# Kernel tuning notes

Hardware: AMD Instinct MI355X
Metric: run time of the kernel (lower is better)

The kernel has to match this reference:

```python
import jax, jax.numpy as jnp
import numpy as np
import math


def _per_component_log_likelihood(x, MU, A, D, PI):
    # x: [N,d]; MU,D: [K,d]; A: [K,d,l]; PI: [K]
    K, d, l = A.shape
    iD = D ** (-2.0)                                   # [K,d]  (1/sigma^2 per feature)
    B = iD[:, :, None] * A                             # [K,d,l] = diag(iD_k) @ A_k
    # L_k = I_l + A_k^T diag(iD_k) A_k  (Woodbury inner matrix)
    L = jnp.eye(l, dtype=x.dtype)[None] + jnp.einsum('kdl,kdm->klm', A, B)
    iL = jnp.linalg.inv(L)                             # [K,l,l]
    # Mahalanobis term m_d[n,k] = xc^T iD xc - (xc^T iD A) iL (A^T iD xc),
    # expanded so we never materialize the [K,N,d] centered tensor.
    t_quad = (x * x) @ iD.T                            # [N,K]
    t_cross = x @ (iD * MU).T                          # [N,K]
    t_const = jnp.sum(iD * MU * MU, axis=1)            # [K]
    term1 = t_quad - 2.0 * t_cross + t_const[None, :]
    y = jnp.einsum('nd,kdl->nkl', x, B) - jnp.einsum('kd,kdl->kl', MU, B)[None]
    term2 = jnp.einsum('nkl,klm,nkm->nk', y, iL, y)
    m_d = term1 - term2                                # [N,K]
    # log|Sigma_k| = log|L_k| - sum_d log iD[k,d]
    log_det_Sigma = jnp.log(jnp.linalg.det(L)) + jnp.sum(jnp.log(D ** 2.0), axis=1)
    log_prob = -0.5 * ((d * math.log(2.0 * math.pi) + log_det_Sigma)[None, :] + m_d)
    # NOTE: faithful to the source, which adds PI (not log PI) here.
    return PI[None, :] + log_prob                      # [N,K]


def setup_inputs() -> dict:
    key = jax.random.key(0)
    k1, k2, k3, k4 = jax.random.split(key, 4)
    N, K, d, l = 500000, 32, 128, 4
    x = jax.random.normal(k1, (N, d), dtype=jnp.float32)
    MU = jax.random.normal(k2, (K, d), dtype=jnp.float32)
    A = 0.1 * jax.random.normal(k3, (K, d, l), dtype=jnp.float32)
    D = jax.random.uniform(k4, (K, d), dtype=jnp.float32, minval=0.5, maxval=1.5)
    PI = jnp.ones((K,), dtype=jnp.float32) / K
    return {"x": x, "MU": MU, "A": A, "D": D, "PI": PI}


def reference(x, MU, A, D, PI):
    comp_ll = _per_component_log_likelihood(x, MU, A, D, PI)   # [N,K]
    return jax.scipy.special.logsumexp(comp_ll, axis=1)        # [N] = MFA.log_prob(x)
```

## Files before the change

kernel.cpp:

```cpp
#include <hip/hip_runtime.h>
#include <hip/hip_bf16.h>

typedef _Float16 half8 __attribute__((ext_vector_type(8)));
typedef float f32x4 __attribute__((ext_vector_type(4)));

#define KC 32
#define DD 128
#define LL 4
#define NCOL 192
#define NBLK 768

__global__ __launch_bounds__(256) void mfa_precompute(
    const float* __restrict__ MU, const float* __restrict__ A,
    const float* __restrict__ D, const float* __restrict__ PI,
    _Float16* __restrict__ wsw, float* __restrict__ wsc, float* __restrict__ wsh)
{
  __shared__ float sPart[KC][8][16];
  __shared__ float sRi[KC][LL][LL];
  const int tid = threadIdx.x;
  const int k = tid >> 3;
  const int sub = tid & 7;

  {
    float p[16];
#pragma unroll
    for (int i = 0; i < 16; ++i) p[i] = 0.f;
    const int d0 = sub * 16;
    for (int di = 0; di < 16; ++di) {
      const int d = d0 + di;
      const float Dv = D[k*DD + d];
      const float id = 1.0f/(Dv*Dv);
      const float mu = MU[k*DD + d];
      float a[LL];
#pragma unroll
      for (int l = 0; l < LL; ++l) a[l] = A[(k*DD + d)*LL + l];
      int s = 0;
#pragma unroll
      for (int l = 0; l < LL; ++l) {
#pragma unroll
        for (int m2 = 0; m2 <= l; ++m2) { p[s] += a[l]*id*a[m2]; ++s; }
        p[10 + l] += mu*id*a[l];
      }
      p[14] += id*mu*mu;
      p[15] += logf(Dv*Dv);
    }
#pragma unroll
    for (int i = 0; i < 16; ++i) sPart[k][sub][i] = p[i];
  }
  __syncthreads();

  if (tid < KC) {
    const int kk = tid;
    float p[16];
#pragma unroll
    for (int i = 0; i < 16; ++i) p[i] = 0.f;
    for (int s = 0; s < 8; ++s)
#pragma unroll
      for (int i = 0; i < 16; ++i) p[i] += sPart[kk][s][i];

    float Lm[LL][LL];
    {
      int s = 0;
      for (int l = 0; l < LL; ++l)
        for (int m2 = 0; m2 <= l; ++m2) { Lm[l][m2] = p[s]; ++s; }
    }
    for (int l = 0; l < LL; ++l) Lm[l][l] += 1.0f;
    float c[LL];
    for (int l = 0; l < LL; ++l) c[l] = p[10 + l];
    const float t_const  = p[14];
    const float sumlogD2 = p[15];

    float Lo[LL][LL];
    for (int i = 0; i < LL; ++i)
      for (int j = 0; j < LL; ++j) Lo[i][j] = 0.f;
    for (int i = 0; i < LL; ++i) {
      float s = Lm[i][i];
      for (int m2 = 0; m2 < i; ++m2) s -= Lo[i][m2]*Lo[i][m2];
      Lo[i][i] = sqrtf(s);
      for (int j = i + 1; j < LL; ++j) {
        float t = Lm[j][i];
        for (int m2 = 0; m2 < i; ++m2) t -= Lo[j][m2]*Lo[i][m2];
        Lo[j][i] = t / Lo[i][i];
      }
    }
    float Ri[LL][LL];
    for (int i = 0; i < LL; ++i)
      for (int j = 0; j < LL; ++j) Ri[i][j] = 0.f;
    for (int i = 0; i < LL; ++i) {
      Ri[i][i] = 1.0f/Lo[i][i];
      for (int j = 0; j < i; ++j) {
        float s = 0.f;
        for (int m2 = j; m2 < i; ++m2) s += Lo[i][m2]*Ri[m2][j];
        Ri[i][j] = -s / Lo[i][i];
      }
    }
    for (int i = 0; i < LL; ++i)
      for (int j = 0; j < LL; ++j) sRi[kk][i][j] = Ri[i][j];
    for (int l = 0; l < LL; ++l) {
      float s = 0.f;
      for (int m2 = 0; m2 <= l; ++m2) s += Ri[l][m2]*c[m2];
      wsh[kk*LL + l] = s;
    }
    float logdetL = 0.f;
    for (int i = 0; i < LL; ++i) logdetL += logf(Lo[i][i]);
    logdetL *= 2.0f;
    const float dlog2pi = 235.24826473f;
    wsc[kk] = PI[kk] - 0.5f*(dlog2pi + logdetL + sumlogD2) - 0.5f*t_const;
  }
  __syncthreads();

  for (int idx = tid; idx < NCOL*DD; idx += blockDim.x) {
    const int j8   = idx & 7;
    const int lane = (idx >> 3) & 63;
    const int s    = (idx >> 9) & 3;
    const int t    = idx >> 11;
    const int col  = t*16 + (lane & 15);
    const int dd   = s*32 + ((lane >> 4) << 3) + j8;
    float v;
    if (col < 32) {
      const float Dv = D[col*DD + dd];
      v = 1.0f/(Dv*Dv);
    } else if (col < 64) {
      const int kk = col - 32;
      const float Dv = D[kk*DD + dd];
      v = MU[kk*DD + dd]/(Dv*Dv);
    } else {
      const int kk = (col - 64) >> 2, l = (col - 64) & 3;
      const float Dv = D[kk*DD + dd];
      const float id = 1.0f/(Dv*Dv);
      float s2 = 0.f;
      for (int m2 = 0; m2 <= l; ++m2) s2 += A[(kk*DD + dd)*LL + m2]*sRi[kk][l][m2];
      v = id*s2;
    }
    wsw[idx] = (_Float16)v;
  }
}

__global__ __launch_bounds__(256, 3) void mfa_main(
    const float* __restrict__ x, const _Float16* __restrict__ wsw,
    const float* __restrict__ wsc, const float* __restrict__ wsh,
    float* __restrict__ out, int N, int ntiles, int iters)
{
  __shared__ int4 sWbuf[3072];
  const int tid = threadIdx.x;

  {
    const int4* src = (const int4*)wsw;
    for (int i = tid; i < 3072; i += 256) sWbuf[i] = src[i];
  }

  const half8* sW8 = (const half8*)sWbuf;
  const int wv = tid >> 6, lane = tid & 63;
  const int m = lane & 15, g = lane >> 4;
  const int q = m >> 2;
  const int gbase = lane & 48;

  const float c0 = wsc[m];
  const float c1 = wsc[16 + m];
  float hh[8];
#pragma unroll
  for (int j = 0; j < 8; ++j) hh[j] = wsh[j*16 + m];

  __syncthreads();

  for (int it = 0; it < iters; ++it) {
    const int tile = it*(NBLK*4) + (int)blockIdx.x*4 + wv;
    if (tile >= ntiles) continue;

    const int row = tile*16 + m;
    const float* xr = x + (size_t)row*DD + g*8;
    half8 ax[4], ax2[4];
#pragma unroll
    for (int s = 0; s < 4; ++s) {
      const float4 v0 = *(const float4*)(xr + s*32);
      const float4 v1 = *(const float4*)(xr + s*32 + 4);
      half8 h, h2;
      h[0] = (_Float16)v0.x; h[1] = (_Float16)v0.y;
      h[2] = (_Float16)v0.z; h[3] = (_Float16)v0.w;
      h[4] = (_Float16)v1.x; h[5] = (_Float16)v1.y;
      h[6] = (_Float16)v1.z; h[7] = (_Float16)v1.w;
      h2[0] = (_Float16)(v0.x*v0.x); h2[1] = (_Float16)(v0.y*v0.y);
      h2[2] = (_Float16)(v0.z*v0.z); h2[3] = (_Float16)(v0.w*v0.w);
      h2[4] = (_Float16)(v1.x*v1.x); h2[5] = (_Float16)(v1.y*v1.y);
      h2[6] = (_Float16)(v1.z*v1.z); h2[7] = (_Float16)(v1.w*v1.w);
      ax[s] = h; ax2[s] = h2;
    }

    f32x4 acc[12];
#pragma unroll
    for (int t = 0; t < 12; ++t)
#pragma unroll
      for (int r = 0; r < 4; ++r) acc[t][r] = 0.f;

#pragma unroll
    for (int s = 0; s < 4; ++s) {
#pragma unroll
      for (int t = 0; t < 12; ++t) {
        const half8 b = sW8[(t*4 + s)*64 + lane];
        acc[t] = __builtin_amdgcn_mfma_f32_16x16x32_f16(
            (t < 2) ? ax2[s] : ax[s], b, acc[t], 0, 0, 0);
      }
    }

    float vp0[4], vp1[4];
#pragma unroll
    for (int r = 0; r < 4; ++r) {
      vp0[r] = acc[2][r] - 0.5f*acc[0][r] + c0;
      vp1[r] = acc[3][r] - 0.5f*acc[1][r] + c1;
    }
    float t2[8][4];
#pragma unroll
    for (int j = 0; j < 8; ++j)
#pragma unroll
      for (int r = 0; r < 4; ++r) {
        float e = acc[j + 4][r] - hh[j];
        e = e*e;
        e += __shfl_xor(e, 1);
        e += __shfl_xor(e, 2);
        t2[j][r] = e;
      }
    float res[4];
#pragma unroll
    for (int r = 0; r < 4; ++r) {
      float v[8];
#pragma unroll
      for (int jj = 0; jj < 4; ++jj) {
        const int src = gbase + 4*jj + q;
        v[jj]     = __shfl(vp0[r], src) + 0.5f*t2[jj][r];
        v[jj + 4] = __shfl(vp1[r], src) + 0.5f*t2[jj + 4][r];
      }
      float mx = v[0];
#pragma unroll
      for (int i = 1; i < 8; ++i) mx = fmaxf(mx, v[i]);
      mx = fmaxf(mx, __shfl_xor(mx, 4));
      mx = fmaxf(mx, __shfl_xor(mx, 8));
      float sum = 0.f;
#pragma unroll
      for (int i = 0; i < 8; ++i) sum += __expf(v[i] - mx);
      sum += __shfl_xor(sum, 4);
      sum += __shfl_xor(sum, 8);
      res[r] = mx + __logf(sum);
    }
    if (m == 0) {
      float4 o; o.x = res[0]; o.y = res[1]; o.z = res[2]; o.w = res[3];
      *(float4*)(out + (size_t)tile*16 + g*4) = o;
    }
  }
}

extern "C" void kernel_launch(void* const* d_in, const int* in_sizes, int n_in,
                              void* d_out, int out_size, void* d_ws, size_t ws_size,
                              hipStream_t stream) {
  const float* x  = (const float*)d_in[0];
  const float* MU = (const float*)d_in[1];
  const float* A  = (const float*)d_in[2];
  const float* D  = (const float*)d_in[3];
  const float* PI = (const float*)d_in[4];
  float* out = (float*)d_out;

  const int N = in_sizes[0] / DD;
  _Float16* wsw = (_Float16*)d_ws;
  float* wsc = (float*)((char*)d_ws + (size_t)NCOL*DD*sizeof(_Float16));
  float* wsh = wsc + KC;

  hipLaunchKernelGGL(mfa_precompute, dim3(1), dim3(256), 0, stream,
                     MU, A, D, PI, wsw, wsc, wsh);

  const int ntiles = (N + 15) / 16;
  const int iters  = (ntiles + NBLK*4 - 1) / (NBLK*4);
  hipLaunchKernelGGL(mfa_main, dim3(NBLK), dim3(256), 0, stream,
                     x, wsw, wsc, wsh, out, N, ntiles, iters);
}
```

Measured before the change: 401.6 us.

## Prefetch next x tile in registers and parallelize weight precompute across blocks

```diff
diff --git a/kernel.cpp b/kernel.cpp
--- a/kernel.cpp
+++ b/kernel.cpp
@@ -9,14 +9,14 @@
 #define LL 4
 #define NCOL 192
 #define NBLK 768
-
-__global__ __launch_bounds__(256) void mfa_precompute(
+#define NSLOT (NBLK*4)
+
+__global__ __launch_bounds__(256) void mfa_woodbury(
     const float* __restrict__ MU, const float* __restrict__ A,
     const float* __restrict__ D, const float* __restrict__ PI,
-    _Float16* __restrict__ wsw, float* __restrict__ wsc, float* __restrict__ wsh)
+    float* __restrict__ wsc, float* __restrict__ wsh, float* __restrict__ wsr)
 {
   __shared__ float sPart[KC][8][16];
-  __shared__ float sRi[KC][LL][LL];
   const int tid = threadIdx.x;
   const int k = tid >> 3;
   const int sub = tid & 7;
@@ -26,6 +26,7 @@
 #pragma unroll
     for (int i = 0; i < 16; ++i) p[i] = 0.f;
     const int d0 = sub * 16;
+#pragma unroll 4
     for (int di = 0; di < 16; ++di) {
       const int d = d0 + di;
       const float Dv = D[k*DD + d];
@@ -42,7 +43,7 @@
         p[10 + l] += mu*id*a[l];
       }
       p[14] += id*mu*mu;
-      p[15] += logf(Dv*Dv);
+      p[15] += __logf(Dv*Dv);
     }
 #pragma unroll
     for (int i = 0; i < 16; ++i) sPart[k][sub][i] = p[i];
@@ -95,45 +96,50 @@
       }
     }
     for (int i = 0; i < LL; ++i)
-      for (int j = 0; j < LL; ++j) sRi[kk][i][j] = Ri[i][j];
+      for (int j = 0; j < LL; ++j) wsr[kk*16 + i*4 + j] = Ri[i][j];
     for (int l = 0; l < LL; ++l) {
       float s = 0.f;
       for (int m2 = 0; m2 <= l; ++m2) s += Ri[l][m2]*c[m2];
       wsh[kk*LL + l] = s;
     }
     float logdetL = 0.f;
-    for (int i = 0; i < LL; ++i) logdetL += logf(Lo[i][i]);
+    for (int i = 0; i < LL; ++i) logdetL += __logf(Lo[i][i]);
     logdetL *= 2.0f;
     const float dlog2pi = 235.24826473f;
     wsc[kk] = PI[kk] - 0.5f*(dlog2pi + logdetL + sumlogD2) - 0.5f*t_const;
   }
-  __syncthreads();
-
-  for (int idx = tid; idx < NCOL*DD; idx += blockDim.x) {
-    const int j8   = idx & 7;
-    const int lane = (idx >> 3) & 63;
-    const int s    = (idx >> 9) & 3;
-    const int t    = idx >> 11;
-    const int col  = t*16 + (lane & 15);
-    const int dd   = s*32 + ((lane >> 4) << 3) + j8;
-    float v;
-    if (col < 32) {
-      const float Dv = D[col*DD + dd];
-      v = 1.0f/(Dv*Dv);
-    } else if (col < 64) {
-      const int kk = col - 32;
-      const float Dv = D[kk*DD + dd];
-      v = MU[kk*DD + dd]/(Dv*Dv);
-    } else {
-      const int kk = (col - 64) >> 2, l = (col - 64) & 3;
-      const float Dv = D[kk*DD + dd];
-      const float id = 1.0f/(Dv*Dv);
-      float s2 = 0.f;
-      for (int m2 = 0; m2 <= l; ++m2) s2 += A[(kk*DD + dd)*LL + m2]*sRi[kk][l][m2];
-      v = id*s2;
-    }
-    wsw[idx] = (_Float16)v;
-  }
+}
+
+__global__ __launch_bounds__(256) void mfa_weights(
+    const float* __restrict__ MU, const float* __restrict__ A,
+    const float* __restrict__ D, const float* __restrict__ wsr,
+    _Float16* __restrict__ wsw)
+{
+  const int idx = (int)blockIdx.x*256 + (int)threadIdx.x;
+  const int j8   = idx & 7;
+  const int lane = (idx >> 3) & 63;
+  const int s    = (idx >> 9) & 3;
+  const int t    = idx >> 11;
+  const int col  = t*16 + (lane & 15);
+  const int dd   = s*32 + ((lane >> 4) << 3) + j8;
+  float v;
+  if (col < 32) {
+    const float Dv = D[col*DD + dd];
+    v = 1.0f/(Dv*Dv);
+  } else if (col < 64) {
+    const int kk = col - 32;
+    const float Dv = D[kk*DD + dd];
+    v = MU[kk*DD + dd]/(Dv*Dv);
+  } else {
+    const int kk = (col - 64) >> 2, l = (col - 64) & 3;
+    const float Dv = D[kk*DD + dd];
+    const float id = 1.0f/(Dv*Dv);
+    float s2 = 0.f;
+    for (int m2 = 0; m2 <= l; ++m2)
+      s2 += A[(kk*DD + dd)*LL + m2] * wsr[kk*16 + l*4 + m2];
+    v = id*s2;
+  }
+  wsw[idx] = (_Float16)v;
 }
 
 __global__ __launch_bounds__(256, 3) void mfa_main(
@@ -163,17 +169,42 @@
 
   __syncthreads();
 
+  int tile = (int)blockIdx.x*4 + wv;
+  const int tmax = ntiles - 1;
+
+  float4 xv[8];
+  {
+    const int t0 = tile < ntiles ? tile : tmax;
+    const float* xr = x + (size_t)(t0*16 + m)*DD + g*8;
+#pragma unroll
+    for (int s = 0; s < 4; ++s) {
+      xv[2*s]     = *(const float4*)(xr + s*32);
+      xv[2*s + 1] = *(const float4*)(xr + s*32 + 4);
+    }
+  }
+
   for (int it = 0; it < iters; ++it) {
-    const int tile = it*(NBLK*4) + (int)blockIdx.x*4 + wv;
-    if (tile >= ntiles) continue;
-
-    const int row = tile*16 + m;
-    const float* xr = x + (size_t)row*DD + g*8;
-    half8 ax[4], ax2[4];
+    const int tnext = tile + NSLOT;
+    float4 xvn[8];
+    {
+      const int tp = tnext < ntiles ? tnext : tmax;
+      const float* xrn = x + (size_t)(tp*16 + m)*DD + g*8;
+#pragma unroll
+      for (int s = 0; s < 4; ++s) {
+        xvn[2*s]     = *(const float4*)(xrn + s*32);
+        xvn[2*s + 1] = *(const float4*)(xrn + s*32 + 4);
+      }
+    }
+
+    f32x4 acc[12];
+#pragma unroll
+    for (int t = 0; t < 12; ++t)
+#pragma unroll
+      for (int r = 0; r < 4; ++r) acc[t][r] = 0.f;
+
 #pragma unroll
     for (int s = 0; s < 4; ++s) {
-      const float4 v0 = *(const float4*)(xr + s*32);
-      const float4 v1 = *(const float4*)(xr + s*32 + 4);
+      const float4 v0 = xv[2*s], v1 = xv[2*s + 1];
       half8 h, h2;
       h[0] = (_Float16)v0.x; h[1] = (_Float16)v0.y;
       h[2] = (_Float16)v0.z; h[3] = (_Float16)v0.w;
@@ -183,22 +214,11 @@
       h2[2] = (_Float16)(v0.z*v0.z); h2[3] = (_Float16)(v0.w*v0.w);
       h2[4] = (_Float16)(v1.x*v1.x); h2[5] = (_Float16)(v1.y*v1.y);
       h2[6] = (_Float16)(v1.z*v1.z); h2[7] = (_Float16)(v1.w*v1.w);
-      ax[s] = h; ax2[s] = h2;
-    }
-
-    f32x4 acc[12];
-#pragma unroll
-    for (int t = 0; t < 12; ++t)
-#pragma unroll
-      for (int r = 0; r < 4; ++r) acc[t][r] = 0.f;
-
-#pragma unroll
-    for (int s = 0; s < 4; ++s) {
 #pragma unroll
       for (int t = 0; t < 12; ++t) {
         const half8 b = sW8[(t*4 + s)*64 + lane];
         acc[t] = __builtin_amdgcn_mfma_f32_16x16x32_f16(
-            (t < 2) ? ax2[s] : ax[s], b, acc[t], 0, 0, 0);
+            (t < 2) ? h2 : h, b, acc[t], 0, 0, 0);
       }
     }
 
@@ -241,10 +261,14 @@
       sum += __shfl_xor(sum, 8);
       res[r] = mx + __logf(sum);
     }
-    if (m == 0) {
+    if (m == 0 && tile < ntiles) {
       float4 o; o.x = res[0]; o.y = res[1]; o.z = res[2]; o.w = res[3];
       *(float4*)(out + (size_t)tile*16 + g*4) = o;
     }
+
+#pragma unroll
+    for (int i = 0; i < 8; ++i) xv[i] = xvn[i];
+    tile = tnext;
   }
 }
 
@@ -262,12 +286,15 @@
   _Float16* wsw = (_Float16*)d_ws;
   float* wsc = (float*)((char*)d_ws + (size_t)NCOL*DD*sizeof(_Float16));
   float* wsh = wsc + KC;
-
-  hipLaunchKernelGGL(mfa_precompute, dim3(1), dim3(256), 0, stream,
-                     MU, A, D, PI, wsw, wsc, wsh);
+  float* wsr = wsh + KC*LL;
+
+  hipLaunchKernelGGL(mfa_woodbury, dim3(1), dim3(256), 0, stream,
+                     MU, A, D, PI, wsc, wsh, wsr);
+  hipLaunchKernelGGL(mfa_weights, dim3(96), dim3(256), 0, stream,
+                     MU, A, D, wsr, wsw);
 
   const int ntiles = (N + 15) / 16;
-  const int iters  = (ntiles + NBLK*4 - 1) / (NBLK*4);
+  const int iters  = (ntiles + NSLOT - 1) / NSLOT;
   hipLaunchKernelGGL(mfa_main, dim3(NBLK), dim3(256), 0, stream,
                      x, wsw, wsc, wsh, out, N, ntiles, iters);
 }
```

Result: slower. 498.2 us (+24.1%).
